# Kernel optimization log

Hardware: AMD Instinct MI355X
Metric: run time of the kernel (lower is better)

The kernel has to match this reference:

```python
import jax, jax.numpy as jnp
import numpy as np

SAMPLES = 300000
B = 256
D = 128
NEG = 1024
TEMP = 0.07
MOMENTUM = 0.5
EPS = 1e-12


def _l2n(x):
    # torch F.normalize(p=2, dim=1) semantics
    n = jnp.sqrt(jnp.sum(x * x, axis=-1, keepdims=True))
    return x / jnp.maximum(n, EPS)


def setup_inputs() -> dict:
    key = jax.random.key(0)
    k1, k2, k3, k4, k5, k6 = jax.random.split(key, 6)
    return {
        "audio_emb": jax.random.normal(k1, (B, D), dtype=jnp.float32),
        "video_emb": jax.random.normal(k2, (B, D), dtype=jnp.float32),
        "audio_memory": _l2n(jax.random.normal(k3, (SAMPLES, D), dtype=jnp.float32)),
        "video_memory": _l2n(jax.random.normal(k4, (SAMPLES, D), dtype=jnp.float32)),
        "indices": jax.random.randint(k5, (B,), 0, SAMPLES, dtype=jnp.int64),
        "neg_samples": jax.random.randint(k6, (B, NEG), 0, SAMPLES - 1, dtype=jnp.int64),
    }


def _scores(ctx, pos, neg):
    # ctx [B,D], pos [B,D], neg [B,NEG,D] -> [B, 1+NEG]
    s_pos = jnp.sum(pos * ctx, axis=-1, keepdims=True) / TEMP           # [B,1]
    s_neg = jnp.einsum("bnd,bd->bn", neg, ctx) / TEMP                   # [B,NEG]
    return jnp.concatenate([s_pos, s_neg], axis=1)


def reference(audio_emb, video_emb, audio_memory, video_memory, indices, neg_samples):
    na = _l2n(audio_emb)  # [B,D]
    nv = _l2n(video_emb)

    # alias sampling over uniform probs == uniform randint; shift to skip positive
    neg_idx = neg_samples + (neg_samples >= indices[:, None]).astype(neg_samples.dtype)

    pos_a = audio_memory[indices]      # [B,D]
    pos_v = video_memory[indices]
    neg_a = audio_memory[neg_idx]      # [B,NEG,D]
    neg_v = video_memory[neg_idx]

    # score order: (inter)audio_video, (inter)video_audio, (intra)audio, (intra)video
    scores = jnp.stack([
        _scores(na, pos_v, neg_v),
        _scores(nv, pos_a, neg_a),
        _scores(na, pos_a, neg_a),
        _scores(nv, pos_v, neg_v),
    ], axis=0)  # [4, B, 1+NEG]

    # momentum memory update (no-grad in original): gather -> mix -> normalize -> scatter
    new_a = _l2n(pos_a * MOMENTUM + na * (1.0 - MOMENTUM))
    new_v = _l2n(pos_v * MOMENTUM + nv * (1.0 - MOMENTUM))
    audio_memory_new = audio_memory.at[indices].set(new_a)
    video_memory_new = video_memory.at[indices].set(new_v)

    return scores, audio_memory_new, video_memory_new
```

## Files before the change

### kernel.cpp

```cpp
#include <hip/hip_runtime.h>

#define B 256
#define D 128
#define NEG 1024
#define SAMPLES 300000
#define TEMP 0.07f
#define EPS 1e-12f

constexpr int SCORES_ELEMS = 4 * B * (NEG + 1);
constexpr int MEM_ELEMS    = SAMPLES * D;

__device__ inline float wave_reduce_sum(float x) {
    #pragma unroll
    for (int off = 32; off > 0; off >>= 1) x += __shfl_xor(x, off, 64);
    return x;
}

__global__ __launch_bounds__(64) void prep_kernel(
    const float* __restrict__ audio_emb, const float* __restrict__ video_emb,
    const float* __restrict__ a_mem, const float* __restrict__ v_mem,
    const int* __restrict__ indices,
    float* __restrict__ na, float* __restrict__ nv,
    float* __restrict__ new_a, float* __restrict__ new_v,
    float* __restrict__ scores)
{
    const int b = blockIdx.x;
    const int l = threadIdx.x;

    float2 a = ((const float2*)(audio_emb + b * D))[l];
    float2 v = ((const float2*)(video_emb + b * D))[l];

    float sa = wave_reduce_sum(a.x * a.x + a.y * a.y);
    float sv = wave_reduce_sum(v.x * v.x + v.y * v.y);
    float ira = 1.0f / fmaxf(sqrtf(sa), EPS);
    float irv = 1.0f / fmaxf(sqrtf(sv), EPS);
    float2 naf = {a.x * ira, a.y * ira};
    float2 nvf = {v.x * irv, v.y * irv};
    ((float2*)(na + b * D))[l] = naf;
    ((float2*)(nv + b * D))[l] = nvf;

    const long long idx = (long long)indices[b];
    float2 pa = ((const float2*)(a_mem + idx * D))[l];
    float2 pv = ((const float2*)(v_mem + idx * D))[l];

    float d0 = wave_reduce_sum(pv.x * naf.x + pv.y * naf.y);
    float d1 = wave_reduce_sum(pa.x * nvf.x + pa.y * nvf.y);
    float d2 = wave_reduce_sum(pa.x * naf.x + pa.y * naf.y);
    float d3 = wave_reduce_sum(pv.x * nvf.x + pv.y * nvf.y);
    if (l == 0) {
        scores[(0 * B + b) * (NEG + 1)] = d0 / TEMP;
        scores[(1 * B + b) * (NEG + 1)] = d1 / TEMP;
        scores[(2 * B + b) * (NEG + 1)] = d2 / TEMP;
        scores[(3 * B + b) * (NEG + 1)] = d3 / TEMP;
    }

    float2 ta = {0.5f * (pa.x + naf.x), 0.5f * (pa.y + naf.y)};
    float2 tv = {0.5f * (pv.x + nvf.x), 0.5f * (pv.y + nvf.y)};
    float sta = wave_reduce_sum(ta.x * ta.x + ta.y * ta.y);
    float stv = wave_reduce_sum(tv.x * tv.x + tv.y * tv.y);
    float irta = 1.0f / fmaxf(sqrtf(sta), EPS);
    float irtv = 1.0f / fmaxf(sqrtf(stv), EPS);
    ta.x *= irta; ta.y *= irta;
    tv.x *= irtv; tv.y *= irtv;
    ((float2*)(new_a + b * D))[l] = ta;
    ((float2*)(new_v + b * D))[l] = tv;
}

__global__ __launch_bounds__(256) void neg_scores_kernel(
    const float* __restrict__ a_mem, const float* __restrict__ v_mem,
    const int* __restrict__ indices, const int* __restrict__ neg_samples,
    const float* __restrict__ na, const float* __restrict__ nv,
    float* __restrict__ scores)
{
    const int b = blockIdx.y;
    const int n = blockIdx.x * blockDim.x + threadIdx.x;

    __shared__ float4 na_s[D / 4];
    __shared__ float4 nv_s[D / 4];
    if (threadIdx.x < D / 4)
        na_s[threadIdx.x] = ((const float4*)(na + b * D))[threadIdx.x];
    else if (threadIdx.x < D / 2)
        nv_s[threadIdx.x - D / 4] = ((const float4*)(nv + b * D))[threadIdx.x - D / 4];
    __syncthreads();

    const int pos = indices[b];
    const int ns  = neg_samples[b * NEG + n];
    const long long ni = (long long)ns + (ns >= pos ? 1 : 0);

    const float4* ra = (const float4*)(a_mem + ni * D);
    const float4* rv = (const float4*)(v_mem + ni * D);

    float s0 = 0.f, s1 = 0.f, s2 = 0.f, s3 = 0.f;
    #pragma unroll
    for (int k = 0; k < D / 4; ++k) {
        float4 A = ra[k];
        float4 V = rv[k];
        float4 NA = na_s[k];
        float4 NV = nv_s[k];
        s0 += V.x * NA.x + V.y * NA.y + V.z * NA.z + V.w * NA.w;
        s1 += A.x * NV.x + A.y * NV.y + A.z * NV.z + A.w * NV.w;
        s2 += A.x * NA.x + A.y * NA.y + A.z * NA.z + A.w * NA.w;
        s3 += V.x * NV.x + V.y * NV.y + V.z * NV.z + V.w * NV.w;
    }
    scores[(0 * B + b) * (NEG + 1) + 1 + n] = s0 / TEMP;
    scores[(1 * B + b) * (NEG + 1) + 1 + n] = s1 / TEMP;
    scores[(2 * B + b) * (NEG + 1) + 1 + n] = s2 / TEMP;
    scores[(3 * B + b) * (NEG + 1) + 1 + n] = s3 / TEMP;
}

__global__ __launch_bounds__(256) void copy_kernel(
    const float4* __restrict__ a_mem, const float4* __restrict__ v_mem,
    float4* __restrict__ out_a, float4* __restrict__ out_v, int n4)
{
    int i = blockIdx.x * blockDim.x + threadIdx.x;
    if (i < n4) {
        out_a[i] = a_mem[i];
    } else {
        i -= n4;
        if (i < n4) out_v[i] = v_mem[i];
    }
}

__global__ __launch_bounds__(128) void scatter_kernel(
    const int* __restrict__ indices,
    const float* __restrict__ new_a, const float* __restrict__ new_v,
    float* __restrict__ out_a, float* __restrict__ out_v)
{
    const int b = blockIdx.x;
    const int t = threadIdx.x;
    const int myidx = indices[b];

    __shared__ int skip;
    if (t == 0) skip = 0;
    __syncthreads();
    for (int b2 = b + 1 + t; b2 < B; b2 += blockDim.x)
        if (indices[b2] == myidx) skip = 1;
    __syncthreads();
    if (skip) return;

    out_a[(long long)myidx * D + t] = new_a[b * D + t];
    out_v[(long long)myidx * D + t] = new_v[b * D + t];
}

extern "C" void kernel_launch(void* const* d_in, const int* in_sizes, int n_in,
                              void* d_out, int out_size, void* d_ws, size_t ws_size,
                              hipStream_t stream) {
    const float* audio_emb   = (const float*)d_in[0];
    const float* video_emb   = (const float*)d_in[1];
    const float* a_mem       = (const float*)d_in[2];
    const float* v_mem       = (const float*)d_in[3];
    const int*   indices     = (const int*)d_in[4];
    const int*   neg_samples = (const int*)d_in[5];

    float* out    = (float*)d_out;
    float* scores = out;
    float* out_a  = out + SCORES_ELEMS;
    float* out_v  = out_a + MEM_ELEMS;

    float* ws    = (float*)d_ws;
    float* na    = ws;
    float* nv    = na + B * D;
    float* new_a = nv + B * D;
    float* new_v = new_a + B * D;

    prep_kernel<<<B, 64, 0, stream>>>(audio_emb, video_emb, a_mem, v_mem, indices,
                                      na, nv, new_a, new_v, scores);

    dim3 g2(NEG / 256, B);
    neg_scores_kernel<<<g2, 256, 0, stream>>>(a_mem, v_mem, indices, neg_samples,
                                              na, nv, scores);

    const int n4 = MEM_ELEMS / 4;
    copy_kernel<<<(2 * n4) / 256, 256, 0, stream>>>((const float4*)a_mem, (const float4*)v_mem,
                                                    (float4*)out_a, (float4*)out_v, n4);

    scatter_kernel<<<B, D, 0, stream>>>(indices, new_a, new_v, out_a, out_v);
}
```

Before: 569.0 us.

## Assign one 32-lane group per negative row for coalesced gathers

The negative-score kernel now gives each gathered memory row to 32 lanes, each loading one float4, and reduces the four dot products with xor shuffles. Before, each thread walked a whole 512-byte row alone, so loads across a wave were uncoalesced. The change launches 32x more blocks and adds shuffle reductions, plus redundant loads of the normalized embeddings, in exchange for contiguous row reads.

```diff
diff --git a/kernel.cpp b/kernel.cpp
--- a/kernel.cpp
+++ b/kernel.cpp
@@ -72,40 +72,38 @@
     const float* __restrict__ na, const float* __restrict__ nv,
     float* __restrict__ scores)
 {
-    const int b = blockIdx.y;
-    const int n = blockIdx.x * blockDim.x + threadIdx.x;
-
-    __shared__ float4 na_s[D / 4];
-    __shared__ float4 nv_s[D / 4];
-    if (threadIdx.x < D / 4)
-        na_s[threadIdx.x] = ((const float4*)(na + b * D))[threadIdx.x];
-    else if (threadIdx.x < D / 2)
-        nv_s[threadIdx.x - D / 4] = ((const float4*)(nv + b * D))[threadIdx.x - D / 4];
-    __syncthreads();
+    const int b    = blockIdx.y;
+    const int hw   = threadIdx.x >> 5;
+    const int lane = threadIdx.x & 31;
+    const int n    = blockIdx.x * 8 + hw;
 
     const int pos = indices[b];
     const int ns  = neg_samples[b * NEG + n];
     const long long ni = (long long)ns + (ns >= pos ? 1 : 0);
 
-    const float4* ra = (const float4*)(a_mem + ni * D);
-    const float4* rv = (const float4*)(v_mem + ni * D);
+    float4 A  = ((const float4*)(a_mem + ni * D))[lane];
+    float4 V  = ((const float4*)(v_mem + ni * D))[lane];
+    float4 NA = ((const float4*)(na + (long long)b * D))[lane];
+    float4 NV = ((const float4*)(nv + (long long)b * D))[lane];
 
-    float s0 = 0.f, s1 = 0.f, s2 = 0.f, s3 = 0.f;
+    float s0 = V.x * NA.x + V.y * NA.y + V.z * NA.z + V.w * NA.w;
+    float s1 = A.x * NV.x + A.y * NV.y + A.z * NV.z + A.w * NV.w;
+    float s2 = A.x * NA.x + A.y * NA.y + A.z * NA.z + A.w * NA.w;
+    float s3 = V.x * NV.x + V.y * NV.y + V.z * NV.z + V.w * NV.w;
+
     #pragma unroll
-    for (int k = 0; k < D / 4; ++k) {
-        float4 A = ra[k];
-        float4 V = rv[k];
-        float4 NA = na_s[k];
-        float4 NV = nv_s[k];
-        s0 += V.x * NA.x + V.y * NA.y + V.z * NA.z + V.w * NA.w;
-        s1 += A.x * NV.x + A.y * NV.y + A.z * NV.z + A.w * NV.w;
-        s2 += A.x * NA.x + A.y * NA.y + A.z * NA.z + A.w * NA.w;
-        s3 += V.x * NV.x + V.y * NV.y + V.z * NV.z + V.w * NV.w;
+    for (int off = 16; off > 0; off >>= 1) {
+        s0 += __shfl_xor(s0, off, 64);
+        s1 += __shfl_xor(s1, off, 64);
+        s2 += __shfl_xor(s2, off, 64);
+        s3 += __shfl_xor(s3, off, 64);
     }
-    scores[(0 * B + b) * (NEG + 1) + 1 + n] = s0 / TEMP;
-    scores[(1 * B + b) * (NEG + 1) + 1 + n] = s1 / TEMP;
-    scores[(2 * B + b) * (NEG + 1) + 1 + n] = s2 / TEMP;
-    scores[(3 * B + b) * (NEG + 1) + 1 + n] = s3 / TEMP;
+    if (lane == 0) {
+        scores[(0 * B + b) * (NEG + 1) + 1 + n] = s0 / TEMP;
+        scores[(1 * B + b) * (NEG + 1) + 1 + n] = s1 / TEMP;
+        scores[(2 * B + b) * (NEG + 1) + 1 + n] = s2 / TEMP;
+        scores[(3 * B + b) * (NEG + 1) + 1 + n] = s3 / TEMP;
+    }
 }
 
 __global__ __launch_bounds__(256) void copy_kernel(
@@ -166,7 +164,7 @@
     prep_kernel<<<B, 64, 0, stream>>>(audio_emb, video_emb, a_mem, v_mem, indices,
                                       na, nv, new_a, new_v, scores);
 
-    dim3 g2(NEG / 256, B);
+    dim3 g2(NEG / 8, B);
     neg_scores_kernel<<<g2, 256, 0, stream>>>(a_mem, v_mem, indices, neg_samples,
                                               na, nv, scores);
 
```

Result: faster. 541.4 us (-4.8%).
